# Optimization experiments

Measured on AMD Instinct MI355X. Metric: run time of the kernel, lower is better.

Reference implementation:

```python
import jax, jax.numpy as jnp
import numpy as np
import math

B, T, D, H = 4, 1024, 1024, 16
DK = D // H
TAU_THRESH = 0.3


def setup_inputs() -> dict:
    key = jax.random.key(0)
    ks = jax.random.split(key, 13)
    s = 1.0 / math.sqrt(D)
    return {
        "x": jax.random.normal(ks[0], (B, T, D), dtype=jnp.float32),
        "Wq": jax.random.normal(ks[1], (D, D), dtype=jnp.float32) * s,
        "bq": jax.random.normal(ks[2], (D,), dtype=jnp.float32) * s,
        "Wk": jax.random.normal(ks[3], (D, D), dtype=jnp.float32) * s,
        "bk": jax.random.normal(ks[4], (D,), dtype=jnp.float32) * s,
        "Wv": jax.random.normal(ks[5], (D, D), dtype=jnp.float32) * s,
        "bv": jax.random.normal(ks[6], (D,), dtype=jnp.float32) * s,
        "Wo": jax.random.normal(ks[7], (D, D), dtype=jnp.float32) * s,
        "bo": jax.random.normal(ks[8], (D,), dtype=jnp.float32) * s,
        "Wg1": jax.random.normal(ks[9], (1, D), dtype=jnp.float32) * s,
        "bg1": jax.random.normal(ks[10], (1,), dtype=jnp.float32) * s,
        "Wg2": jax.random.normal(ks[11], (1, D), dtype=jnp.float32) * s,
        "bg2": jax.random.normal(ks[12], (1,), dtype=jnp.float32) * s,
    }


def reference(x, Wq, bq, Wk, bk, Wv, bv, Wo, bo, Wg1, bg1, Wg2, bg2):
    b, t, d = x.shape
    # projections (torch Linear: y = x @ W.T + b)
    Q = (x @ Wq.T + bq).reshape(b, t, H, DK).transpose(0, 2, 1, 3)  # [B,H,T,dk]
    K = (x @ Wk.T + bk).reshape(b, t, H, DK).transpose(0, 2, 1, 3)
    V = (x @ Wv.T + bv).reshape(b, t, H, DK).transpose(0, 2, 1, 3)
    scores = jnp.einsum("bhqd,bhkd->bhqk", Q, K) / math.sqrt(DK)  # [B,H,T,T]
    # confidence gates from first-token query context [B, H*dk] = [B, D]
    context = Q[:, :, 0, :].reshape(b, d)
    q1 = jax.nn.sigmoid(context @ Wg1.T + bg1)  # [B,1]
    q2 = jax.nn.sigmoid(context @ Wg2.T + bg2)  # [B,1]
    c = jnp.clip(q1 * q2, 1e-8, 1.0)            # [B,1]
    tau = jnp.where(c < TAU_THRESH, 1.0 / c, jnp.ones_like(c)).reshape(b, 1, 1, 1)
    p = jax.nn.softmax(scores / tau, axis=-1)
    cb = c.reshape(b, 1, 1, 1)
    p_gated = cb * p + (1.0 - cb) * (1.0 / t)
    u = jnp.mean(1.0 - c, axis=-1, keepdims=True)  # [B,1]
    attn_out = jnp.einsum("bhqk,bhkd->bhqd", p_gated, V)
    attn_out = attn_out.transpose(0, 2, 1, 3).reshape(b, t, d)
    output = attn_out @ Wo.T + bo
    return output, u
```

## Files before the change

### kernel.cpp

```cpp
#include <hip/hip_runtime.h>
#include <stdint.h>

typedef short bf16x8 __attribute__((ext_vector_type(8)));
typedef float f32x4 __attribute__((ext_vector_type(4)));

#define MFMA_BF16(a, b, c) __builtin_amdgcn_mfma_f32_16x16x32_bf16((a), (b), (c), 0, 0, 0)

__device__ __forceinline__ short f2bf(float x) {
  union { float f; uint32_t u; } v; v.f = x;
  uint32_t r = (v.u + 0x7FFFu + ((v.u >> 16) & 1u)) >> 16;
  return (short)r;
}
__device__ __forceinline__ uint32_t rnd_bf_hi(float x) {
  union { float f; uint32_t u; } v; v.f = x;
  return v.u + 0x7FFFu + ((v.u >> 16) & 1u);
}
__device__ __forceinline__ uint32_t pack2bf(float a, float b) {
  return __builtin_amdgcn_perm(rnd_bf_hi(b), rnd_bf_hi(a), 0x07060302);
}
__device__ __forceinline__ float bfbits2f(uint32_t b16) {
  union { uint32_t u; float f; } v; v.u = b16 << 16; return v.f;
}
__device__ __forceinline__ float fexp2(float x) {
#if __has_builtin(__builtin_amdgcn_exp2f)
  return __builtin_amdgcn_exp2f(x);
#else
  return __expf(x * 0.6931471805599453f);
#endif
}
__device__ __forceinline__ void async16(const void* g, void* l) {
  __builtin_amdgcn_global_load_lds(
      (const __attribute__((address_space(1))) uint32_t*)g,
      (__attribute__((address_space(3))) uint32_t*)l, 16, 0, 0);
}

#define BAR() __builtin_amdgcn_s_barrier()
#define LGKM0() asm volatile("s_waitcnt lgkmcnt(0)" ::: "memory")
#define VMCNT(n) asm volatile("s_waitcnt vmcnt(" #n ")" ::: "memory")
#define PRIO1() __builtin_amdgcn_s_setprio(1)
#define PRIO0() __builtin_amdgcn_s_setprio(0)

__global__ __launch_bounds__(256) void prep_k(
    const float* __restrict__ x, const float* __restrict__ Wq,
    const float* __restrict__ Wk, const float* __restrict__ Wv,
    const float* __restrict__ Wo, const float* __restrict__ bq,
    short* __restrict__ xb, short* __restrict__ Wqb, short* __restrict__ Wkb,
    short* __restrict__ Wvb, short* __restrict__ Wob, float* __restrict__ ctx) {
  __shared__ float xs[1024];
  const int bid = blockIdx.x;
  const int tid = threadIdx.x;
  if (bid < 8192) {
    const float* src; short* dst; int idx;
    if (bid < 4096) {
      src = x; dst = xb; idx = (bid << 8) + tid;
    } else {
      const int r = bid - 4096;
      const int z = r >> 10;
      src = (z == 0) ? Wq : (z == 1) ? Wk : (z == 2) ? Wv : Wo;
      dst = (z == 0) ? Wqb : (z == 1) ? Wkb : (z == 2) ? Wvb : Wob;
      idx = ((r & 1023) << 8) + tid;
    }
    float4 v = ((const float4*)src)[idx];
    short4 o;
    o.x = f2bf(v.x); o.y = f2bf(v.y); o.z = f2bf(v.z); o.w = f2bf(v.w);
    ((short4*)dst)[idx] = o;
  } else {
    const int r = bid - 8192;
    const int b = r >> 4;
    const int n0 = (r & 15) << 6;
    for (int i = tid; i < 1024; i += 256) xs[i] = x[b * 1048576 + i];
    __syncthreads();
    const int w = tid >> 6, lane = tid & 63;
    const float4* xv4 = (const float4*)xs;
    for (int rr = 0; rr < 16; ++rr) {
      const int n = n0 + (w << 4) + rr;
      const float4* wrow = (const float4*)(Wq + n * 1024);
      float p = 0.f;
#pragma unroll
      for (int c2 = 0; c2 < 4; ++c2) {
        float4 wv = wrow[lane + (c2 << 6)];
        float4 xv = xv4[lane + (c2 << 6)];
        p += xv.x * wv.x + xv.y * wv.y + xv.z * wv.z + xv.w * wv.w;
      }
#pragma unroll
      for (int off = 32; off; off >>= 1) p += __shfl_xor(p, off);
      if (lane == 0) ctx[b * 1024 + n] = p + bq[n];
    }
  }
}

__global__ __launch_bounds__(256) void gates_fin(const float* __restrict__ ctx,
                                                 const float* __restrict__ Wg1,
                                                 const float* __restrict__ bg1,
                                                 const float* __restrict__ Wg2,
                                                 const float* __restrict__ bg2,
                                                 float* __restrict__ gates,
                                                 float* __restrict__ u_out) {
  __shared__ float red[16];
  const int tid = threadIdx.x, w = tid >> 6, lane = tid & 63;
  for (int b = 0; b < 4; ++b) {
    float4 cv = ((const float4*)(ctx + b * 1024))[tid];
    float4 w1 = ((const float4*)Wg1)[tid];
    float4 w2 = ((const float4*)Wg2)[tid];
    float p1 = cv.x * w1.x + cv.y * w1.y + cv.z * w1.z + cv.w * w1.w;
    float p2 = cv.x * w2.x + cv.y * w2.y + cv.z * w2.z + cv.w * w2.w;
#pragma unroll
    for (int off = 32; off; off >>= 1) { p1 += __shfl_xor(p1, off); p2 += __shfl_xor(p2, off); }
    if (lane == 0) { red[w] = p1; red[8 + w] = p2; }
    __syncthreads();
    if (tid == 0) {
      float g1 = red[0] + red[1] + red[2] + red[3] + bg1[0];
      float g2 = red[8] + red[9] + red[10] + red[11] + bg2[0];
      float q1 = 1.f / (1.f + expf(-g1));
      float q2 = 1.f / (1.f + expf(-g2));
      float c = fminf(fmaxf(q1 * q2, 1e-8f), 1.0f);
      gates[b * 2 + 0] = c;
      gates[b * 2 + 1] = (c < 0.3f ? c : 1.0f) * 0.125f * 1.4426950408889634f;
      u_out[b] = 1.0f - c;
    }
    __syncthreads();
  }
}

template <bool SWP>
__device__ __forceinline__ void qkv_core(const short* __restrict__ xb,
                                         const short* __restrict__ W,
                                         const float* __restrict__ bias,
                                         short* __restrict__ out,
                                         short* sm, int m0, int nl0) {
  const int tid = threadIdx.x;
  const int wid = tid >> 6, lane = tid & 63;
  const int wr = wid >> 2, wc = wid & 3;
  const int m15 = lane & 15, quad = lane >> 4;
  const int swz = m15 & 7;

  const int rowb = tid >> 3;
  const int cs = ((tid & 7) ^ (rowb & 7)) << 3;
  const short* aB = xb + (m0 + rowb) * 1024 + cs;
  const short* bB = W + (nl0 + rowb) * 1024 + cs;

  short* As = sm;
  short* Bs = sm + 32768;

#define STAGEH(sb, tt, hf, dst)                        \
  do {                                                 \
    const short* _s = (sb) + (hf)*131072 + (tt)*64;    \
    short* _d = (dst) + ((hf) << 13) + (tid << 3);     \
    async16(_s, _d);                                   \
    async16(_s + 65536, _d + 4096);                    \
  } while (0)

#define RD(base, f, kk)                                                        \
  (*(const bf16x8*)((base) + ((f) << 10) + (m15 << 6) +                        \
                    (((((kk) << 2) + quad) ^ swz) << 3)))

#define MM(accr, af, bf)                                   \
  do {                                                     \
    if (SWP) accr = MFMA_BF16((bf), (af), (accr));         \
    else     accr = MFMA_BF16((af), (bf), (accr));         \
  } while (0)

  f32x4 acc[8][4];
#pragma unroll
  for (int i = 0; i < 8; ++i)
#pragma unroll
    for (int j = 0; j < 4; ++j) { f32x4 zz = {0.f, 0.f, 0.f, 0.f}; acc[i][j] = zz; }

  STAGEH(bB, 0, 0, Bs);
  STAGEH(aB, 0, 0, As);
  STAGEH(aB, 0, 1, As);
  STAGEH(bB, 0, 1, Bs);
  STAGEH(bB, 1, 0, Bs + 16384);
  STAGEH(aB, 1, 0, As + 16384);
  VMCNT(4);
  BAR();

  bf16x8 a[4][2], b0[2][2], b1[2][2];

  for (int t = 0; t < 16; ++t) {
    const int buf = t & 1;
    const short* Ab = As + (buf << 14) + (wr << 13);
    const short* Bb = Bs + (buf << 14) + ((wc >> 1) << 13) + ((wc & 1) << 12);
    short* Adn = As + ((buf ^ 1) << 14);
    short* Bdn = Bs + ((buf ^ 1) << 14);
    short* Ad2 = As + (buf << 14);
    short* Bd2 = Bs + (buf << 14);

#pragma unroll
    for (int fi = 0; fi < 4; ++fi) { a[fi][0] = RD(Ab, fi, 0); a[fi][1] = RD(Ab, fi, 1); }
#pragma unroll
    for (int fj = 0; fj < 2; ++fj) { b0[fj][0] = RD(Bb, fj, 0); b0[fj][1] = RD(Bb, fj, 1); }
    if (t < 15) STAGEH(aB, t + 1, 1, Adn);
    BAR();
    LGKM0();
    PRIO1();
#pragma unroll
    for (int fi = 0; fi < 4; ++fi)
#pragma unroll
      for (int fj = 0; fj < 2; ++fj) {
        MM(acc[fi][fj], a[fi][0], b0[fj][0]);
        MM(acc[fi][fj], a[fi][1], b0[fj][1]);
      }
    PRIO0();
    BAR();

#pragma unroll
    for (int fj = 0; fj < 2; ++fj) { b1[fj][0] = RD(Bb, 2 + fj, 0); b1[fj][1] = RD(Bb, 2 + fj, 1); }
    if (t < 15) STAGEH(bB, t + 1, 1, Bdn);
    BAR();
    LGKM0();
    PRIO1();
#pragma unroll
    for (int fi = 0; fi < 4; ++fi)
#pragma unroll
      for (int fj = 0; fj < 2; ++fj) {
        MM(acc[fi][2 + fj], a[fi][0], b1[fj][0]);
        MM(acc[fi][2 + fj], a[fi][1], b1[fj][1]);
      }
    PRIO0();
    BAR();

#pragma unroll
    for (int fi = 0; fi < 4; ++fi) { a[fi][0] = RD(Ab, 4 + fi, 0); a[fi][1] = RD(Ab, 4 + fi, 1); }
    if (t < 14) STAGEH(bB, t + 2, 0, Bd2);
    BAR();
    LGKM0();
    PRIO1();
#pragma unroll
    for (int fi = 0; fi < 4; ++fi)
#pragma unroll
      for (int fj = 0; fj < 2; ++fj) {
        MM(acc[4 + fi][2 + fj], a[fi][0], b1[fj][0]);
        MM(acc[4 + fi][2 + fj], a[fi][1], b1[fj][1]);
      }
    PRIO0();
    BAR();

    if (t < 14) STAGEH(aB, t + 2, 0, Ad2);
    BAR();
    PRIO1();
#pragma unroll
    for (int fi = 0; fi < 4; ++fi)
#pragma unroll
      for (int fj = 0; fj < 2; ++fj) {
        MM(acc[4 + fi][fj], a[fi][0], b0[fj][0]);
        MM(acc[4 + fi][fj], a[fi][1], b0[fj][1]);
      }
    PRIO0();
    if (t < 14) { VMCNT(4); }
    else if (t == 14) { VMCNT(0); }
    BAR();
  }

  const int nw = nl0 + (wc << 6);
  if (SWP) {
#pragma unroll
    for (int fj = 0; fj < 4; ++fj) {
      const int n = nw + (fj << 4) + (quad << 2);
      const float4 bv = *(const float4*)(bias + n);
      const int hh = n >> 6, dk0 = n & 63;
#pragma unroll
      for (int fi = 0; fi < 8; ++fi) {
        const int m = m0 + (wr << 7) + (fi << 4) + m15;
        const int bb = m >> 10, tt = m & 1023;
        uint2 st;
        st.x = pack2bf(acc[fi][fj][0] + bv.x, acc[fi][fj][1] + bv.y);
        st.y = pack2bf(acc[fi][fj][2] + bv.z, acc[fi][fj][3] + bv.w);
        *(uint2*)(out + (((bb << 4) + hh) << 16) + (tt << 6) + dk0) = st;
      }
    }
  } else {
#pragma unroll
    for (int fj = 0; fj < 4; ++fj) {
      const int n = nw + (fj << 4) + m15;
      const float bv = bias[n];
      const int hh = n >> 6, dk = n & 63;
#pragma unroll
      for (int fi = 0; fi < 8; ++fi) {
        const int m = m0 + (wr << 7) + (fi << 4) + (quad << 2);
        const int bb = m >> 10, t0 = m & 1023;
        uint2 st;
        st.x = pack2bf(acc[fi][fj][0] + bv, acc[fi][fj][1] + bv);
        st.y = pack2bf(acc[fi][fj][2] + bv, acc[fi][fj][3] + bv);
        *(uint2*)(out + (((bb << 4) + hh) << 16) + (dk << 10) + t0) = st;
      }
    }
  }
#undef STAGEH
#undef RD
#undef MM
}

__global__ __launch_bounds__(512) void gemm_qkv8(
    const short* __restrict__ xb,
    const short* __restrict__ Wqb, const short* __restrict__ Wkb, const short* __restrict__ Wvb,
    const float* __restrict__ bq, const float* __restrict__ bk, const float* __restrict__ bv,
    short* __restrict__ Qh, short* __restrict__ Kh, short* __restrict__ Vt) {
  const int lin = blockIdx.x;
  const int s = ((lin & 7) * 24) + (lin >> 3);
  const int bx = s & 15, by = s >> 4;
  const int z = by >> 2;
  const int m0 = bx << 8, nl0 = (by & 3) << 8;
  extern __shared__ short sm[];
  if (z == 0)      qkv_core<true >(xb, Wqb, bq, Qh, sm, m0, nl0);
  else if (z == 1) qkv_core<true >(xb, Wkb, bk, Kh, sm, m0, nl0);
  else             qkv_core<false>(xb, Wvb, bv, Vt, sm, m0, nl0);
}

__global__ __launch_bounds__(256) void gemm_out(const short* __restrict__ Ab,
                                                const short* __restrict__ Wo,
                                                const float* __restrict__ bo,
                                                float* __restrict__ Cout) {
  const int m0 = blockIdx.x << 7;
  const int n0 = blockIdx.y << 7;
  const int tid = threadIdx.x;
  const int w = tid >> 6, lane = tid & 63;
  const int m15 = lane & 15, quad = lane >> 4;
  const int wr = w >> 1, wc = w & 1;

  __shared__ short As[4096];
  __shared__ short Bs[4096];

  f32x4 acc[4][4];
#pragma unroll
  for (int i = 0; i < 4; ++i)
#pragma unroll
    for (int j = 0; j < 4; ++j) { f32x4 zz = {0.f, 0.f, 0.f, 0.f}; acc[i][j] = zz; }

  const int srow = (w << 5) + (lane >> 2);
  const int scol = (lane & 3) << 3;
  const short* ga0 = Ab + (m0 + srow) * 1024 + scol;
  const short* ga1 = ga0 + 16 * 1024;
  const short* gb0 = Wo + (n0 + srow) * 1024 + scol;
  const short* gb1 = gb0 + 16 * 1024;
  short* la0 = &As[srow * 32 + scol];
  short* la1 = la0 + 512;
  short* lb0 = &Bs[srow * 32 + scol];
  short* lb1 = lb0 + 512;

  for (int kt = 0; kt < 32; ++kt) {
    async16(ga0, la0); async16(ga1, la1);
    async16(gb0, lb0); async16(gb1, lb1);
    ga0 += 32; ga1 += 32; gb0 += 32; gb1 += 32;
    __syncthreads();
    bf16x8 a[4], b[4];
#pragma unroll
    for (int i = 0; i < 4; ++i)
      a[i] = *(const bf16x8*)(&As[((wr << 6) + (i << 4) + m15) * 32 + (quad << 3)]);
#pragma unroll
    for (int j = 0; j < 4; ++j)
      b[j] = *(const bf16x8*)(&Bs[((wc << 6) + (j << 4) + m15) * 32 + (quad << 3)]);
#pragma unroll
    for (int i = 0; i < 4; ++i)
#pragma unroll
      for (int j = 0; j < 4; ++j)
        acc[i][j] = MFMA_BF16(a[i], b[j], acc[i][j]);
    __syncthreads();
  }

#pragma unroll
  for (int j = 0; j < 4; ++j) {
    const int n = n0 + (wc << 6) + (j << 4) + m15;
    const float bb_ = bo[n];
#pragma unroll
    for (int i = 0; i < 4; ++i) {
      const int mb = m0 + (wr << 6) + (i << 4) + (quad << 2);
#pragma unroll
      for (int r = 0; r < 4; ++r)
        Cout[(mb + r) * 1024 + n] = acc[i][j][r] + bb_;
    }
  }
}

__global__ __launch_bounds__(256, 2) void attn_k(const short* __restrict__ Qh,
                                                 const short* __restrict__ Kh,
                                                 const short* __restrict__ Vt,
                                                 const float* __restrict__ gates,
                                                 short* __restrict__ attnb) {
  const int bh = blockIdx.x;
  const int b = bh >> 4, h = bh & 15;
  const int q0 = blockIdx.y << 7;
  const int tid = threadIdx.x;
  const int w = tid >> 6, lane = tid & 63;
  const int m15 = lane & 15, quad = lane >> 4;

  __shared__ short Ks[2][4096];
  __shared__ short Vs[3][4096];

  const short* ksrc = Kh + bh * 65536;
  const short* vsrc = Vt + bh * 65536;

  const float sl = gates[b * 2 + 1];

  const short* qsrcA = Qh + ((bh << 10) + q0 + (w << 4) + m15) * 64;
  const short* qsrcB = qsrcA + 64 * 64;
  const bf16x8 qA0 = *(const bf16x8*)(qsrcA + (quad << 3));
  const bf16x8 qA1 = *(const bf16x8*)(qsrcA + 32 + (quad << 3));
  const bf16x8 qB0 = *(const bf16x8*)(qsrcB + (quad << 3));
  const bf16x8 qB1 = *(const bf16x8*)(qsrcB + 32 + (quad << 3));

  const bf16x8 vone = {0x3F80, 0x3F80, 0x3F80, 0x3F80, 0x3F80, 0x3F80, 0x3F80, 0x3F80};

  const int off0 = tid, off1 = tid + 256;
  const int r0 = off0 >> 3, cb0 = (off0 & 7) ^ (r0 & 7);
  const int r1 = off1 >> 3, cb1 = (off1 & 7) ^ (r1 & 7);

#define STAGE(kv, kb, vb)                                                      \
  do {                                                                         \
    async16(ksrc + (((kv) << 6) + r0) * 64 + (cb0 << 3), &Ks[kb][off0 << 3]);  \
    async16(ksrc + (((kv) << 6) + r1) * 64 + (cb1 << 3), &Ks[kb][off1 << 3]);  \
    async16(vsrc + r0 * 1024 + ((kv) << 6) + (cb0 << 3), &Vs[vb][off0 << 3]);  \
    async16(vsrc + r1 * 1024 + ((kv) << 6) + (cb1 << 3), &Vs[vb][off1 << 3]);  \
  } while (0)

  STAGE(0, 0, 0);

  float lsumA = 0.f, lsumB = 0.f;
  f32x4 oA[4], oB[4], o_mv[4];
#pragma unroll
  for (int jd = 0; jd < 4; ++jd) {
    f32x4 zz = {0.f, 0.f, 0.f, 0.f};
    oA[jd] = zz; oB[jd] = zz; o_mv[jd] = zz;
  }

  const int srcA = ((quad & 1) << 5) + m15;
  const int srcB = srcA + 16;
  const bool selhi = (quad & 2) != 0;

#define BUILD_PF(pf, pk)                                                       \
  do {                                                                         \
    _Pragma("unroll")                                                          \
    for (int Hh = 0; Hh < 2; ++Hh) {                                           \
      uint32_t f[4];                                                           \
      _Pragma("unroll")                                                        \
      for (int rp = 0; rp < 2; ++rp) {                                         \
        uint32_t alo = (uint32_t)__shfl((int)pk[2 * Hh][rp], srcA);            \
        uint32_t ahi = (uint32_t)__shfl((int)pk[2 * Hh + 1][rp], srcA);        \
        uint32_t blo = (uint32_t)__shfl((int)pk[2 * Hh][rp], srcB);            \
        uint32_t bhi = (uint32_t)__shfl((int)pk[2 * Hh + 1][rp], srcB);        \
        f[rp]     = selhi ? ahi : alo;                                         \
        f[2 + rp] = selhi ? bhi : blo;                                         \
      }                                                                        \
      pf[Hh] = *(bf16x8*)f;                                                    \
    }                                                                          \
  } while (0)

#define PV_STEP(Vb, pfa, pfb)                                                  \
  do {                                                                         \
    _Pragma("unroll")                                                          \
    for (int jd = 0; jd < 4; ++jd) {                                           \
      const int row = (jd << 4) + m15;                                         \
      const int sw = row & 7;                                                  \
      bf16x8 v0 = *(const bf16x8*)((Vb) + (row << 6) + ((quad ^ sw) << 3));    \
      bf16x8 v1 = *(const bf16x8*)((Vb) + (row << 6) + (((quad + 4) ^ sw) << 3)); \
      oA[jd] = MFMA_BF16(v0, pfa[0], oA[jd]);                                  \
      oA[jd] = MFMA_BF16(v1, pfa[1], oA[jd]);                                  \
      oB[jd] = MFMA_BF16(v0, pfb[0], oB[jd]);                                  \
      oB[jd] = MFMA_BF16(v1, pfb[1], oB[jd]);                                  \
      o_mv[jd] = MFMA_BF16(v0, vone, o_mv[jd]);                                \
      o_mv[jd] = MFMA_BF16(v1, vone, o_mv[jd]);                                \
    }                                                                          \
  } while (0)

  bf16x8 pfpA[2], pfpB[2];
  pfpA[0] = (bf16x8){0,0,0,0,0,0,0,0}; pfpA[1] = pfpA[0];
  pfpB[0] = pfpA[0]; pfpB[1] = pfpA[0];

  for (int kv = 0; kv < 16; ++kv) {
    __syncthreads();
    if (kv < 15) STAGE(kv + 1, (kv + 1) & 1, (kv + 1) % 3);
    const short* Kb = &Ks[kv & 1][0];

    f32x4 sA[4], sB[4];
#pragma unroll
    for (int s = 0; s < 4; ++s) {
      const int row = (s << 4) + m15;
      const int sw = row & 7;
      bf16x8 a0 = *(const bf16x8*)(Kb + (row << 6) + ((quad ^ sw) << 3));
      bf16x8 a1 = *(const bf16x8*)(Kb + (row << 6) + (((quad + 4) ^ sw) << 3));
      f32x4 zA = {0.f, 0.f, 0.f, 0.f};
      zA = MFMA_BF16(a0, qA0, zA);
      zA = MFMA_BF16(a1, qA1, zA);
      sA[s] = zA;
      f32x4 zB = {0.f, 0.f, 0.f, 0.f};
      zB = MFMA_BF16(a0, qB0, zB);
      zB = MFMA_BF16(a1, qB1, zB);
      sB[s] = zB;
    }

    if (kv > 0) {
      const short* Vb = &Vs[(kv - 1) % 3][0];
      PV_STEP(Vb, pfpA, pfpB);
    }

    uint32_t pkA[4][2], pkB[4][2];
#pragma unroll
    for (int s = 0; s < 4; ++s) {
      float a0 = fexp2(sA[s][0] * sl);
      float a1 = fexp2(sA[s][1] * sl);
      float a2 = fexp2(sA[s][2] * sl);
      float a3 = fexp2(sA[s][3] * sl);
      lsumA += (a0 + a1) + (a2 + a3);
      pkA[s][0] = pack2bf(a0, a1);
      pkA[s][1] = pack2bf(a2, a3);
      float b0 = fexp2(sB[s][0] * sl);
      float b1 = fexp2(sB[s][1] * sl);
      float b2 = fexp2(sB[s][2] * sl);
      float b3 = fexp2(sB[s][3] * sl);
      lsumB += (b0 + b1) + (b2 + b3);
      pkB[s][0] = pack2bf(b0, b1);
      pkB[s][1] = pack2bf(b2, b3);
    }

    bf16x8 pfA[2], pfB[2];
    BUILD_PF(pfA, pkA);
    BUILD_PF(pfB, pkB);
    pfpA[0] = pfA[0]; pfpA[1] = pfA[1];
    pfpB[0] = pfB[0]; pfpB[1] = pfB[1];
  }

  {
    const short* Vb = &Vs[15 % 3][0];
    PV_STEP(Vb, pfpA, pfpB);
  }
#undef STAGE
#undef BUILD_PF
#undef PV_STEP

  float lA = lsumA;
  lA += __shfl_xor(lA, 16);
  lA += __shfl_xor(lA, 32);
  float lB = lsumB;
  lB += __shfl_xor(lB, 16);
  lB += __shfl_xor(lB, 32);

  const float cg = gates[b * 2 + 0];
  const float sc0A = cg / lA;
  const float sc0B = cg / lB;
  const float coef = (1.0f - cg) * (1.0f / 1024.0f);
  const int qrowA = q0 + (w << 4) + m15;
  short* orowA = attnb + ((b << 10) + qrowA) * 1024 + (h << 6);
  short* orowB = orowA + 64 * 1024;
#pragma unroll
  for (int jd = 0; jd < 4; ++jd) {
    uint2 stA;
    stA.x = pack2bf(sc0A * oA[jd][0] + coef * o_mv[jd][0],
                    sc0A * oA[jd][1] + coef * o_mv[jd][1]);
    stA.y = pack2bf(sc0A * oA[jd][2] + coef * o_mv[jd][2],
                    sc0A * oA[jd][3] + coef * o_mv[jd][3]);
    *(uint2*)(orowA + (jd << 4) + (quad << 2)) = stA;
    uint2 stB;
    stB.x = pack2bf(sc0B * oB[jd][0] + coef * o_mv[jd][0],
                    sc0B * oB[jd][1] + coef * o_mv[jd][1]);
    stB.y = pack2bf(sc0B * oB[jd][2] + coef * o_mv[jd][2],
                    sc0B * oB[jd][3] + coef * o_mv[jd][3]);
    *(uint2*)(orowB + (jd << 4) + (quad << 2)) = stB;
  }
}

extern "C" void kernel_launch(void* const* d_in, const int* in_sizes, int n_in,
                              void* d_out, int out_size, void* d_ws, size_t ws_size,
                              hipStream_t stream) {
  const float* x   = (const float*)d_in[0];
  const float* Wq  = (const float*)d_in[1];
  const float* bq  = (const float*)d_in[2];
  const float* Wk  = (const float*)d_in[3];
  const float* bk  = (const float*)d_in[4];
  const float* Wv  = (const float*)d_in[5];
  const float* bv  = (const float*)d_in[6];
  const float* Wo  = (const float*)d_in[7];
  const float* bo  = (const float*)d_in[8];
  const float* Wg1 = (const float*)d_in[9];
  const float* bg1 = (const float*)d_in[10];
  const float* Wg2 = (const float*)d_in[11];
  const float* bg2 = (const float*)d_in[12];
  float* out = (float*)d_out;

  char* ws = (char*)d_ws;
  short* xb   = (short*)(ws + 0);
  short* Wqb  = (short*)(ws + 8388608);
  short* Wkb  = (short*)(ws + 10485760);
  short* Wvb  = (short*)(ws + 12582912);
  short* Wob  = (short*)(ws + 14680064);
  short* Qh   = (short*)(ws + 16777216);
  short* Kh   = (short*)(ws + 25165824);
  short* Vt   = (short*)(ws + 33554432);
  short* attb = (short*)(ws + 41943040);
  float* ctx  = (float*)(ws + 50331648);
  float* gat  = (float*)(ws + 50348032);

  static bool lds_inited = false;
  if (!lds_inited) {
    hipFuncSetAttribute(reinterpret_cast<const void*>(gemm_qkv8),
                        hipFuncAttributeMaxDynamicSharedMemorySize, 131072);
    lds_inited = true;
  }

  prep_k<<<8256, 256, 0, stream>>>(x, Wq, Wk, Wv, Wo, bq,
                                   xb, Wqb, Wkb, Wvb, Wob, ctx);
  gates_fin<<<1, 256, 0, stream>>>(ctx, Wg1, bg1, Wg2, bg2, gat, out + 4194304);

  gemm_qkv8<<<192, 512, 131072, stream>>>(xb, Wqb, Wkb, Wvb, bq, bk, bv,
                                          Qh, Kh, Vt);
  attn_k<<<dim3(64, 8), 256, 0, stream>>>(Qh, Kh, Vt, gat, attb);
  gemm_out<<<dim3(32, 8), 256, 0, stream>>>(attb, Wob, bo, out);
}
```

Baseline: 209.6 us.

## Replace 256x256 pipelined QKV GEMM with simple 128x128 tiled kernel plus LDS swizzle

Swaps the hand-scheduled 256x256-tile, 512-thread, double-buffered QKV projection kernel (128 KB dynamic LDS, barrier/priority choreography) for a simpler 128x128-tile, 256-thread kernel with 16 KB static LDS and a 3D grid of 768 blocks. The aim is more blocks per CU for occupancy and latency hiding instead of explicit software pipelining. It also adds an XOR swizzle on LDS columns in both the QKV and output GEMMs to reduce bank conflicts on fragment reads. In exchange it gives up double buffering and accepts lower per-block data reuse and more global traffic.

Result: slower. 215.0 us (+2.6%).

```diff
diff --git a/kernel.cpp b/kernel.cpp
--- a/kernel.cpp
+++ b/kernel.cpp
@@ -33,12 +33,6 @@
       (const __attribute__((address_space(1))) uint32_t*)g,
       (__attribute__((address_space(3))) uint32_t*)l, 16, 0, 0);
 }
-
-#define BAR() __builtin_amdgcn_s_barrier()
-#define LGKM0() asm volatile("s_waitcnt lgkmcnt(0)" ::: "memory")
-#define VMCNT(n) asm volatile("s_waitcnt vmcnt(" #n ")" ::: "memory")
-#define PRIO1() __builtin_amdgcn_s_setprio(1)
-#define PRIO0() __builtin_amdgcn_s_setprio(0)
 
 __global__ __launch_bounds__(256) void prep_k(
     const float* __restrict__ x, const float* __restrict__ Wq,
@@ -123,188 +117,106 @@
 }
 
 template <bool SWP>
-__device__ __forceinline__ void qkv_core(const short* __restrict__ xb,
-                                         const short* __restrict__ W,
-                                         const float* __restrict__ bias,
-                                         short* __restrict__ out,
-                                         short* sm, int m0, int nl0) {
+__device__ __forceinline__ void qkv_core128(
+    const short* __restrict__ A, const short* __restrict__ W,
+    const float* __restrict__ bias, short* __restrict__ out,
+    short* As, short* Bs, int m0, int n0) {
   const int tid = threadIdx.x;
-  const int wid = tid >> 6, lane = tid & 63;
-  const int wr = wid >> 2, wc = wid & 3;
+  const int w = tid >> 6, lane = tid & 63;
   const int m15 = lane & 15, quad = lane >> 4;
-  const int swz = m15 & 7;
-
-  const int rowb = tid >> 3;
-  const int cs = ((tid & 7) ^ (rowb & 7)) << 3;
-  const short* aB = xb + (m0 + rowb) * 1024 + cs;
-  const short* bB = W + (nl0 + rowb) * 1024 + cs;
-
-  short* As = sm;
-  short* Bs = sm + 32768;
-
-#define STAGEH(sb, tt, hf, dst)                        \
-  do {                                                 \
-    const short* _s = (sb) + (hf)*131072 + (tt)*64;    \
-    short* _d = (dst) + ((hf) << 13) + (tid << 3);     \
-    async16(_s, _d);                                   \
-    async16(_s + 65536, _d + 4096);                    \
-  } while (0)
-
-#define RD(base, f, kk)                                                        \
-  (*(const bf16x8*)((base) + ((f) << 10) + (m15 << 6) +                        \
-                    (((((kk) << 2) + quad) ^ swz) << 3)))
-
-#define MM(accr, af, bf)                                   \
-  do {                                                     \
-    if (SWP) accr = MFMA_BF16((bf), (af), (accr));         \
-    else     accr = MFMA_BF16((af), (bf), (accr));         \
-  } while (0)
-
-  f32x4 acc[8][4];
-#pragma unroll
-  for (int i = 0; i < 8; ++i)
+  const int wr = w >> 1, wc = w & 1;
+
+  f32x4 acc[4][4];
+#pragma unroll
+  for (int i = 0; i < 4; ++i)
 #pragma unroll
     for (int j = 0; j < 4; ++j) { f32x4 zz = {0.f, 0.f, 0.f, 0.f}; acc[i][j] = zz; }
 
-  STAGEH(bB, 0, 0, Bs);
-  STAGEH(aB, 0, 0, As);
-  STAGEH(aB, 0, 1, As);
-  STAGEH(bB, 0, 1, Bs);
-  STAGEH(bB, 1, 0, Bs + 16384);
-  STAGEH(aB, 1, 0, As + 16384);
-  VMCNT(4);
-  BAR();
-
-  bf16x8 a[4][2], b0[2][2], b1[2][2];
-
-  for (int t = 0; t < 16; ++t) {
-    const int buf = t & 1;
-    const short* Ab = As + (buf << 14) + (wr << 13);
-    const short* Bb = Bs + (buf << 14) + ((wc >> 1) << 13) + ((wc & 1) << 12);
-    short* Adn = As + ((buf ^ 1) << 14);
-    short* Bdn = Bs + ((buf ^ 1) << 14);
-    short* Ad2 = As + (buf << 14);
-    short* Bd2 = Bs + (buf << 14);
-
-#pragma unroll
-    for (int fi = 0; fi < 4; ++fi) { a[fi][0] = RD(Ab, fi, 0); a[fi][1] = RD(Ab, fi, 1); }
-#pragma unroll
-    for (int fj = 0; fj < 2; ++fj) { b0[fj][0] = RD(Bb, fj, 0); b0[fj][1] = RD(Bb, fj, 1); }
-    if (t < 15) STAGEH(aB, t + 1, 1, Adn);
-    BAR();
-    LGKM0();
-    PRIO1();
-#pragma unroll
-    for (int fi = 0; fi < 4; ++fi)
-#pragma unroll
-      for (int fj = 0; fj < 2; ++fj) {
-        MM(acc[fi][fj], a[fi][0], b0[fj][0]);
-        MM(acc[fi][fj], a[fi][1], b0[fj][1]);
+  const int srow = (w << 5) + (lane >> 2);
+  const int sxor = (srow >> 1) & 3;
+  const int scol = (((lane & 3) ^ sxor) << 3);
+  const short* ga0 = A + (m0 + srow) * 1024 + scol;
+  const short* ga1 = ga0 + 16 * 1024;
+  const short* gb0 = W + (n0 + srow) * 1024 + scol;
+  const short* gb1 = gb0 + 16 * 1024;
+  short* la0 = &As[srow * 32 + ((lane & 3) << 3)];
+  short* la1 = la0 + 512;
+  short* lb0 = &Bs[srow * 32 + ((lane & 3) << 3)];
+  short* lb1 = lb0 + 512;
+
+  for (int kt = 0; kt < 32; ++kt) {
+    async16(ga0, la0); async16(ga1, la1);
+    async16(gb0, lb0); async16(gb1, lb1);
+    ga0 += 32; ga1 += 32; gb0 += 32; gb1 += 32;
+    __syncthreads();
+    bf16x8 a[4], b[4];
+#pragma unroll
+    for (int i = 0; i < 4; ++i) {
+      const int ra = (wr << 6) + (i << 4) + m15;
+      a[i] = *(const bf16x8*)(&As[ra * 32 + ((quad ^ ((ra >> 1) & 3)) << 3)]);
+    }
+#pragma unroll
+    for (int j = 0; j < 4; ++j) {
+      const int rb = (wc << 6) + (j << 4) + m15;
+      b[j] = *(const bf16x8*)(&Bs[rb * 32 + ((quad ^ ((rb >> 1) & 3)) << 3)]);
+    }
+#pragma unroll
+    for (int i = 0; i < 4; ++i)
+#pragma unroll
+      for (int j = 0; j < 4; ++j) {
+        if (SWP) acc[i][j] = MFMA_BF16(b[j], a[i], acc[i][j]);
+        else     acc[i][j] = MFMA_BF16(a[i], b[j], acc[i][j]);
       }
-    PRIO0();
-    BAR();
-
-#pragma unroll
-    for (int fj = 0; fj < 2; ++fj) { b1[fj][0] = RD(Bb, 2 + fj, 0); b1[fj][1] = RD(Bb, 2 + fj, 1); }
-    if (t < 15) STAGEH(bB, t + 1, 1, Bdn);
-    BAR();
-    LGKM0();
-    PRIO1();
-#pragma unroll
-    for (int fi = 0; fi < 4; ++fi)
-#pragma unroll
-      for (int fj = 0; fj < 2; ++fj) {
-        MM(acc[fi][2 + fj], a[fi][0], b1[fj][0]);
-        MM(acc[fi][2 + fj], a[fi][1], b1[fj][1]);
-      }
-    PRIO0();
-    BAR();
-
-#pragma unroll
-    for (int fi = 0; fi < 4; ++fi) { a[fi][0] = RD(Ab, 4 + fi, 0); a[fi][1] = RD(Ab, 4 + fi, 1); }
-    if (t < 14) STAGEH(bB, t + 2, 0, Bd2);
-    BAR();
-    LGKM0();
-    PRIO1();
-#pragma unroll
-    for (int fi = 0; fi < 4; ++fi)
-#pragma unroll
-      for (int fj = 0; fj < 2; ++fj) {
-        MM(acc[4 + fi][2 + fj], a[fi][0], b1[fj][0]);
-        MM(acc[4 + fi][2 + fj], a[fi][1], b1[fj][1]);
-      }
-    PRIO0();
-    BAR();
-
-    if (t < 14) STAGEH(aB, t + 2, 0, Ad2);
-    BAR();
-    PRIO1();
-#pragma unroll
-    for (int fi = 0; fi < 4; ++fi)
-#pragma unroll
-      for (int fj = 0; fj < 2; ++fj) {
-        MM(acc[4 + fi][fj], a[fi][0], b0[fj][0]);
-        MM(acc[4 + fi][fj], a[fi][1], b0[fj][1]);
-      }
-    PRIO0();
-    if (t < 14) { VMCNT(4); }
-    else if (t == 14) { VMCNT(0); }
-    BAR();
-  }
-
-  const int nw = nl0 + (wc << 6);
+    __syncthreads();
+  }
+
   if (SWP) {
 #pragma unroll
-    for (int fj = 0; fj < 4; ++fj) {
-      const int n = nw + (fj << 4) + (quad << 2);
+    for (int j = 0; j < 4; ++j) {
+      const int n = n0 + (wc << 6) + (j << 4) + (quad << 2);
       const float4 bv = *(const float4*)(bias + n);
       const int hh = n >> 6, dk0 = n & 63;
 #pragma unroll
-      for (int fi = 0; fi < 8; ++fi) {
-        const int m = m0 + (wr << 7) + (fi << 4) + m15;
+      for (int i = 0; i < 4; ++i) {
+        const int m = m0 + (wr << 6) + (i << 4) + m15;
         const int bb = m >> 10, tt = m & 1023;
         uint2 st;
-        st.x = pack2bf(acc[fi][fj][0] + bv.x, acc[fi][fj][1] + bv.y);
-        st.y = pack2bf(acc[fi][fj][2] + bv.z, acc[fi][fj][3] + bv.w);
+        st.x = pack2bf(acc[i][j][0] + bv.x, acc[i][j][1] + bv.y);
+        st.y = pack2bf(acc[i][j][2] + bv.z, acc[i][j][3] + bv.w);
         *(uint2*)(out + (((bb << 4) + hh) << 16) + (tt << 6) + dk0) = st;
       }
     }
   } else {
 #pragma unroll
-    for (int fj = 0; fj < 4; ++fj) {
-      const int n = nw + (fj << 4) + m15;
+    for (int j = 0; j < 4; ++j) {
+      const int n = n0 + (wc << 6) + (j << 4) + m15;
       const float bv = bias[n];
       const int hh = n >> 6, dk = n & 63;
 #pragma unroll
-      for (int fi = 0; fi < 8; ++fi) {
-        const int m = m0 + (wr << 7) + (fi << 4) + (quad << 2);
+      for (int i = 0; i < 4; ++i) {
+        const int m = m0 + (wr << 6) + (i << 4) + (quad << 2);
         const int bb = m >> 10, t0 = m & 1023;
         uint2 st;
-        st.x = pack2bf(acc[fi][fj][0] + bv, acc[fi][fj][1] + bv);
-        st.y = pack2bf(acc[fi][fj][2] + bv, acc[fi][fj][3] + bv);
+        st.x = pack2bf(acc[i][j][0] + bv, acc[i][j][1] + bv);
+        st.y = pack2bf(acc[i][j][2] + bv, acc[i][j][3] + bv);
         *(uint2*)(out + (((bb << 4) + hh) << 16) + (dk << 10) + t0) = st;
       }
     }
   }
-#undef STAGEH
-#undef RD
-#undef MM
-}
-
-__global__ __launch_bounds__(512) void gemm_qkv8(
+}
+
+__global__ __launch_bounds__(256) void gemm_qkv(
     const short* __restrict__ xb,
     const short* __restrict__ Wqb, const short* __restrict__ Wkb, const short* __restrict__ Wvb,
     const float* __restrict__ bq, const float* __restrict__ bk, const float* __restrict__ bv,
     short* __restrict__ Qh, short* __restrict__ Kh, short* __restrict__ Vt) {
-  const int lin = blockIdx.x;
-  const int s = ((lin & 7) * 24) + (lin >> 3);
-  const int bx = s & 15, by = s >> 4;
-  const int z = by >> 2;
-  const int m0 = bx << 8, nl0 = (by & 3) << 8;
-  extern __shared__ short sm[];
-  if (z == 0)      qkv_core<true >(xb, Wqb, bq, Qh, sm, m0, nl0);
-  else if (z == 1) qkv_core<true >(xb, Wkb, bk, Kh, sm, m0, nl0);
-  else             qkv_core<false>(xb, Wvb, bv, Vt, sm, m0, nl0);
+  __shared__ short As[4096];
+  __shared__ short Bs[4096];
+  const int z = blockIdx.z;
+  const int m0 = blockIdx.x << 7, n0 = blockIdx.y << 7;
+  if (z == 0)      qkv_core128<true >(xb, Wqb, bq, Qh, As, Bs, m0, n0);
+  else if (z == 1) qkv_core128<true >(xb, Wkb, bk, Kh, As, Bs, m0, n0);
+  else             qkv_core128<false>(xb, Wvb, bv, Vt, As, Bs, m0, n0);
 }
 
 __global__ __launch_bounds__(256) void gemm_out(const short* __restrict__ Ab,
@@ -328,14 +240,15 @@
     for (int j = 0; j < 4; ++j) { f32x4 zz = {0.f, 0.f, 0.f, 0.f}; acc[i][j] = zz; }
 
   const int srow = (w << 5) + (lane >> 2);
-  const int scol = (lane & 3) << 3;
+  const int sxor = (srow >> 1) & 3;
+  const int scol = (((lane & 3) ^ sxor) << 3);
   const short* ga0 = Ab + (m0 + srow) * 1024 + scol;
   const short* ga1 = ga0 + 16 * 1024;
   const short* gb0 = Wo + (n0 + srow) * 1024 + scol;
   const short* gb1 = gb0 + 16 * 1024;
-  short* la0 = &As[srow * 32 + scol];
+  short* la0 = &As[srow * 32 + ((lane & 3) << 3)];
   short* la1 = la0 + 512;
-  short* lb0 = &Bs[srow * 32 + scol];
+  short* lb0 = &Bs[srow * 32 + ((lane & 3) << 3)];
   short* lb1 = lb0 + 512;
 
   for (int kt = 0; kt < 32; ++kt) {
@@ -345,11 +258,15 @@
     __syncthreads();
     bf16x8 a[4], b[4];
 #pragma unroll
-    for (int i = 0; i < 4; ++i)
-      a[i] = *(const bf16x8*)(&As[((wr << 6) + (i << 4) + m15) * 32 + (quad << 3)]);
-#pragma unroll
-    for (int j = 0; j < 4; ++j)
-      b[j] = *(const bf16x8*)(&Bs[((wc << 6) + (j << 4) + m15) * 32 + (quad << 3)]);
+    for (int i = 0; i < 4; ++i) {
+      const int ra = (wr << 6) + (i << 4) + m15;
+      a[i] = *(const bf16x8*)(&As[ra * 32 + ((quad ^ ((ra >> 1) & 3)) << 3)]);
+    }
+#pragma unroll
+    for (int j = 0; j < 4; ++j) {
+      const int rb = (wc << 6) + (j << 4) + m15;
+      b[j] = *(const bf16x8*)(&Bs[rb * 32 + ((quad ^ ((rb >> 1) & 3)) << 3)]);
+    }
 #pragma unroll
     for (int i = 0; i < 4; ++i)
 #pragma unroll
@@ -589,19 +506,12 @@
   float* ctx  = (float*)(ws + 50331648);
   float* gat  = (float*)(ws + 50348032);
 
-  static bool lds_inited = false;
-  if (!lds_inited) {
-    hipFuncSetAttribute(reinterpret_cast<const void*>(gemm_qkv8),
-                        hipFuncAttributeMaxDynamicSharedMemorySize, 131072);
-    lds_inited = true;
-  }
-
   prep_k<<<8256, 256, 0, stream>>>(x, Wq, Wk, Wv, Wo, bq,
                                    xb, Wqb, Wkb, Wvb, Wob, ctx);
   gates_fin<<<1, 256, 0, stream>>>(ctx, Wg1, bg1, Wg2, bg2, gat, out + 4194304);
 
-  gemm_qkv8<<<192, 512, 131072, stream>>>(xb, Wqb, Wkb, Wvb, bq, bk, bv,
-                                          Qh, Kh, Vt);
+  gemm_qkv<<<dim3(32, 8, 3), 256, 0, stream>>>(xb, Wqb, Wkb, Wvb, bq, bk, bv,
+                                               Qh, Kh, Vt);
   attn_k<<<dim3(64, 8), 256, 0, stream>>>(Qh, Kh, Vt, gat, attb);
   gemm_out<<<dim3(32, 8), 256, 0, stream>>>(attb, Wob, bo, out);
 }
```
